# Kernel tuning notes

Measured on AMD Instinct MI355X. Metric: run time of the kernel, lower is better.

Reference implementation:

```python
import jax, jax.numpy as jnp
import numpy as np


def _rope_cache(seq_len, head_dim):
    half = head_dim // 2
    inv_freq = 1.0 / (10000.0 ** (jnp.arange(half, dtype=jnp.float32) / half))
    ang = jnp.arange(seq_len, dtype=jnp.float32)[:, None] * inv_freq[None, :]  # [S, half]
    return jnp.cos(ang), jnp.sin(ang)


def _apply_rope(x, cos, sin):
    # x: [B,H,S,D], interleaved pairs (even=x1, odd=x2)
    b, h, s, d = x.shape
    xp = x.reshape(b, h, s, d // 2, 2)
    x1, x2 = xp[..., 0], xp[..., 1]
    c = cos[:s][None, None]
    sn = sin[:s][None, None]
    o1 = x1 * c - x2 * sn
    o2 = x1 * sn + x2 * c
    return jnp.stack([o1, o2], axis=-1).reshape(b, h, s, d)


def setup_inputs() -> dict:
    key = jax.random.key(0)
    ks = jax.random.split(key, 5)
    B, N, D = 2, 2048, 2048
    sc = 0.02
    return {
        "x": jax.random.normal(ks[0], (B, N, D), jnp.float32),
        "wq": jax.random.normal(ks[1], (D, D), jnp.float32) * sc,
        "wk": jax.random.normal(ks[2], (D, D), jnp.float32) * sc,
        "wv": jax.random.normal(ks[3], (D, D), jnp.float32) * sc,
        "wo": jax.random.normal(ks[4], (D, D), jnp.float32) * sc,
    }


def reference(x, wq, wk, wv, wo):
    H = 16
    B, N, D = x.shape
    dk = D // H
    # torch nn.Linear: y = x @ W^T
    def proj(w):
        return (x @ w.T).reshape(B, N, H, dk).transpose(0, 2, 1, 3)  # [B,H,N,dk]
    Q, K, V = proj(wq), proj(wk), proj(wv)
    cos, sin = _rope_cache(N, dk)
    Q = _apply_rope(Q, cos, sin)
    K = _apply_rope(K, cos, sin)
    scores = jnp.einsum('bhnd,bhmd->bhnm', Q, K) / jnp.sqrt(jnp.float32(dk))
    causal = jnp.tril(jnp.ones((N, N), dtype=bool))
    scores = jnp.where(causal[None, None], scores, -jnp.inf)
    attn = jax.nn.softmax(scores, axis=-1)
    out = jnp.einsum('bhnm,bhmd->bhnd', attn, V)
    out = out.transpose(0, 2, 1, 3).reshape(B, N, D)
    return out @ wo.T, K, V
```

## Files before the change

kernel.cpp:

```cpp
#include <hip/hip_runtime.h>
#include <stdint.h>

typedef __bf16 bf16x8 __attribute__((ext_vector_type(8)));
typedef float f32x4 __attribute__((ext_vector_type(4)));

#define DEV __device__ __forceinline__
#define CAST_G(p) (const __attribute__((address_space(1))) unsigned int*)(p)
#define CAST_L(p) (__attribute__((address_space(3))) unsigned int*)(p)

constexpr int SEQ = 2048;
constexpr int DIM = 2048;
constexpr int NH  = 16;
constexpr int DK  = 128;
constexpr int BATCH = 2;
constexpr size_t TSZ = (size_t)BATCH * SEQ * DIM;
constexpr size_t WSZ = (size_t)DIM * DIM;
constexpr float ATTN_SCALE = 0.08838834764831845f;

DEV unsigned short f2bf(float f) {
  unsigned int u = __float_as_uint(f);
  unsigned int r = (u + 0x7fffu + ((u >> 16) & 1u)) >> 16;
  return (unsigned short)r;
}

__global__ __launch_bounds__(256)
void cvt_f32_bf16(const float* __restrict__ src, unsigned short* __restrict__ dst,
                  int n8) {
  int i = blockIdx.x * 256 + threadIdx.x;
  if (i >= n8) return;
  float4 a = *reinterpret_cast<const float4*>(src + (size_t)i * 8);
  float4 b = *reinterpret_cast<const float4*>(src + (size_t)i * 8 + 4);
  unsigned short o[8];
  o[0] = f2bf(a.x); o[1] = f2bf(a.y); o[2] = f2bf(a.z); o[3] = f2bf(a.w);
  o[4] = f2bf(b.x); o[5] = f2bf(b.y); o[6] = f2bf(b.z); o[7] = f2bf(b.w);
  *reinterpret_cast<uint4*>(dst + (size_t)i * 8) = *reinterpret_cast<const uint4*>(o);
}

template <int MODE>
__global__ __launch_bounds__(256, 2)
void gemm_rope(const unsigned short* __restrict__ A,
               const unsigned short* __restrict__ W,
               unsigned short* __restrict__ Db,
               float* __restrict__ Df) {
  __shared__ __align__(16) unsigned short As[128 * 64];
  __shared__ __align__(16) unsigned short Bs[128 * 64];

  const int t = threadIdx.x;
  const int lane = t & 63;
  const int wid = t >> 6;
  const int wr = (wid >> 1) << 6;
  const int wc = (wid & 1) << 6;
  const int l16 = lane & 15, lg = lane >> 4;
  const int row0 = blockIdx.y * 128;
  const int col0 = blockIdx.x * 128;

  const int srow = t >> 3;
  const int scol = ((t & 7) ^ (srow & 7)) << 3;
  const unsigned short* Asrc = A + (size_t)(row0 + srow) * DIM + scol;
  const unsigned short* Wsrc = W + (size_t)(col0 + srow) * DIM + scol;

  f32x4 acc[4][4] = {};

  for (int k0 = 0; k0 < DIM; k0 += 64) {
    __syncthreads();
#pragma unroll
    for (int i = 0; i < 4; ++i) {
      __builtin_amdgcn_global_load_lds(CAST_G(Asrc + (size_t)i * 32 * DIM + k0),
                                       CAST_L(As + i * 2048 + wid * 512), 16, 0, 0);
      __builtin_amdgcn_global_load_lds(CAST_G(Wsrc + (size_t)i * 32 * DIM + k0),
                                       CAST_L(Bs + i * 2048 + wid * 512), 16, 0, 0);
    }
    __syncthreads();
#pragma unroll
    for (int ks = 0; ks < 2; ++ks) {
      bf16x8 af[4], bfr[4];
#pragma unroll
      for (int i = 0; i < 4; ++i) {
        int ra = wr + i * 16 + l16;
        af[i] = *reinterpret_cast<const bf16x8*>(&As[ra * 64 + (((ks * 4 + lg) ^ (ra & 7)) << 3)]);
        int rb = wc + i * 16 + l16;
        bfr[i] = *reinterpret_cast<const bf16x8*>(&Bs[rb * 64 + (((ks * 4 + lg) ^ (rb & 7)) << 3)]);
      }
#pragma unroll
      for (int i = 0; i < 4; ++i)
#pragma unroll
        for (int j = 0; j < 4; ++j)
          acc[i][j] = __builtin_amdgcn_mfma_f32_16x16x32_bf16(af[i], bfr[j], acc[i][j], 0, 0, 0);
    }
  }

  if (MODE == 0) {
#pragma unroll
    for (int i = 0; i < 4; ++i)
#pragma unroll
      for (int j = 0; j < 4; ++j) {
        int colg = col0 + wc + j * 16 + l16;
#pragma unroll
        for (int r = 0; r < 4; ++r) {
          int rowg = row0 + wr + i * 16 + lg * 4 + r;
          Df[(size_t)rowg * DIM + colg] = acc[i][j][r];
        }
      }
  } else {
#pragma unroll
    for (int j = 0; j < 4; ++j) {
      int colg = col0 + wc + j * 16 + l16;
      int jj = (colg >> 1) & 63;
      float invf = __expf((float)jj * -0.14391156831212787f);
#pragma unroll
      for (int i = 0; i < 4; ++i) {
#pragma unroll
        for (int r = 0; r < 4; ++r) {
          int rowg = row0 + wr + i * 16 + lg * 4 + r;
          float v = acc[i][j][r];
          float outv;
          if (MODE == 1 || MODE == 2) {
            float p = __shfl_xor(v, 1, 64);
            int pos = rowg & (SEQ - 1);
            float ang = (float)pos * invf;
            float sn, cs;
            __sincosf(ang, &sn, &cs);
            outv = (colg & 1) ? fmaf(p, sn, v * cs) : fmaf(v, cs, -(p * sn));
          } else {
            outv = v;
          }
          int b = rowg >> 11, pos = rowg & (SEQ - 1);
          int h = colg >> 7, d = colg & (DK - 1);
          size_t idx = (((size_t)(b * NH + h)) * SEQ + pos) * DK + d;
          if (MODE == 1) Db[idx] = f2bf(outv);
          if (MODE == 2) { Df[idx] = outv; Db[idx] = f2bf(outv); }
          if (MODE == 3) Df[idx] = outv;
        }
      }
    }
  }
}

__global__ __launch_bounds__(256, 2)
void vtrans(const float* __restrict__ V, unsigned short* __restrict__ VT) {
  __shared__ float vs[64 * 128];
  const int t = threadIdx.x;
  const int bh = blockIdx.y;
  const int p0 = blockIdx.x * 64;
  const float* src = V + ((size_t)bh * SEQ + p0) * DK;
#pragma unroll
  for (int s = 0; s < 8; ++s) {
    int id = s * 256 + t;
    *reinterpret_cast<float4*>(&vs[id * 4]) = *reinterpret_cast<const float4*>(&src[id * 4]);
  }
  __syncthreads();
  const int w = t >> 6, l = t & 63;
  unsigned short* dstb = VT + (size_t)bh * DK * SEQ + p0;
#pragma unroll
  for (int it = 0; it < 4; ++it) {
    int d = w * 32 + (it & 1) * 16 + (l & 15);
    int kc = (it >> 1) * 4 + (l >> 4);
    unsigned short tmp[8];
#pragma unroll
    for (int j = 0; j < 8; ++j) tmp[j] = f2bf(vs[(kc * 8 + j) * DK + d]);
    *reinterpret_cast<uint4*>(&dstb[(size_t)d * SEQ + kc * 8]) =
        *reinterpret_cast<const uint4*>(tmp);
  }
}

struct __align__(16) AttnSmem {
  unsigned short Qs[128 * 128];
  unsigned short Ks[64 * 128];
  unsigned short Vts[128 * 64];
  unsigned short Ps[8 * 16 * 64];
};

__global__ __launch_bounds__(512, 1)
void attn_fused(const unsigned short* __restrict__ Q,
                const unsigned short* __restrict__ K,
                const unsigned short* __restrict__ VT,
                unsigned short* __restrict__ AO) {
  __shared__ AttnSmem sm;
  const int t = threadIdx.x;
  const int lane = t & 63;
  const int wid = t >> 6;
  const int l16 = lane & 15, lg = lane >> 4;
  const int pj = blockIdx.x;
  const int bh = blockIdx.y;
  const int b = bh >> 4, h = bh & 15;

  const unsigned short* Kbase = K + (size_t)bh * SEQ * DK;
  const unsigned short* VTbase = VT + (size_t)bh * DK * SEQ;

  for (int half = 0; half < 2; ++half) {
    const int qt = half ? pj : (15 - pj);
    const int q0 = qt * 128;
    const int nkv = 2 * (qt + 1);
    const unsigned short* Qbase = Q + ((size_t)bh * SEQ + q0) * DK;

#pragma unroll
    for (int s = 0; s < 4; ++s) {
      int id = s * 512 + t;
      int r = id >> 4, c = id & 15;
      uint4 v = *reinterpret_cast<const uint4*>(Qbase + (size_t)r * DK + (c << 3));
      *reinterpret_cast<uint4*>(&sm.Qs[r * 128 + ((c ^ (r & 7)) << 3)]) = v;
    }

    f32x4 accO[8] = {};
    float mrun[4], lrun[4];
#pragma unroll
    for (int r = 0; r < 4; ++r) { mrun[r] = -INFINITY; lrun[r] = 0.f; }

    uint4 pk[2], pv[2];
#pragma unroll
    for (int s = 0; s < 2; ++s) {
      int id = s * 512 + t;
      int rk = id >> 4, ck = id & 15;
      pk[s] = *reinterpret_cast<const uint4*>(Kbase + (size_t)rk * DK + (ck << 3));
      int rv = id >> 3, cv = id & 7;
      pv[s] = *reinterpret_cast<const uint4*>(VTbase + (size_t)rv * SEQ + (cv << 3));
    }

    for (int kt = 0; kt < nkv; ++kt) {
      const int key0 = kt * 64;
      __syncthreads();
#pragma unroll
      for (int s = 0; s < 2; ++s) {
        int id = s * 512 + t;
        int rk = id >> 4, ck = id & 15;
        *reinterpret_cast<uint4*>(&sm.Ks[rk * 128 + ((ck ^ (rk & 7)) << 3)]) = pk[s];
        int rv = id >> 3, cv = id & 7;
        *reinterpret_cast<uint4*>(&sm.Vts[rv * 64 + ((cv ^ (rv & 7)) << 3)]) = pv[s];
      }
      __syncthreads();
      if (kt + 1 < nkv) {
        const int kn = key0 + 64;
#pragma unroll
        for (int s = 0; s < 2; ++s) {
          int id = s * 512 + t;
          int rk = id >> 4, ck = id & 15;
          pk[s] = *reinterpret_cast<const uint4*>(Kbase + (size_t)(kn + rk) * DK + (ck << 3));
          int rv = id >> 3, cv = id & 7;
          pv[s] = *reinterpret_cast<const uint4*>(VTbase + (size_t)rv * SEQ + kn + (cv << 3));
        }
      }

      f32x4 sf[4] = {};
#pragma unroll
      for (int ks = 0; ks < 4; ++ks) {
        int ra = wid * 16 + l16;
        bf16x8 aq = *reinterpret_cast<const bf16x8*>(
            &sm.Qs[ra * 128 + (((ks * 4 + lg) ^ (ra & 7)) << 3)]);
#pragma unroll
        for (int nj = 0; nj < 4; ++nj) {
          int rb = nj * 16 + l16;
          bf16x8 bk = *reinterpret_cast<const bf16x8*>(
              &sm.Ks[rb * 128 + (((ks * 4 + lg) ^ (rb & 7)) << 3)]);
          sf[nj] = __builtin_amdgcn_mfma_f32_16x16x32_bf16(aq, bk, sf[nj], 0, 0, 0);
        }
      }

      const int qwbase = q0 + wid * 16;
      const bool need_mask = (key0 + 63) > qwbase;
#pragma unroll
      for (int nj = 0; nj < 4; ++nj) {
        int kcol = key0 + nj * 16 + l16;
#pragma unroll
        for (int r = 0; r < 4; ++r) {
          float v = sf[nj][r] * ATTN_SCALE;
          if (need_mask) {
            int qrow = qwbase + lg * 4 + r;
            if (kcol > qrow) v = -INFINITY;
          }
          sf[nj][r] = v;
        }
      }

      float alpha[4];
#pragma unroll
      for (int r = 0; r < 4; ++r) {
        float m0 = fmaxf(fmaxf(sf[0][r], sf[1][r]), fmaxf(sf[2][r], sf[3][r]));
#pragma unroll
        for (int off = 1; off < 16; off <<= 1)
          m0 = fmaxf(m0, __shfl_xor(m0, off, 64));
        float mn = fmaxf(mrun[r], m0);
        alpha[r] = __expf(mrun[r] - mn);
        mrun[r] = mn;
      }
      float rs[4] = {0.f, 0.f, 0.f, 0.f};
#pragma unroll
      for (int nj = 0; nj < 4; ++nj) {
        int colb = nj * 16 + l16;
        int ch = colb >> 3, cb = colb & 7;
#pragma unroll
        for (int r = 0; r < 4; ++r) {
          float p = __expf(sf[nj][r] - mrun[r]);
          rs[r] += p;
          int prow = lg * 4 + r;
          sm.Ps[wid * 1024 + prow * 64 + ((ch ^ (prow & 7)) << 3) + cb] = f2bf(p);
        }
      }
#pragma unroll
      for (int r = 0; r < 4; ++r) {
        float s0 = rs[r];
#pragma unroll
        for (int off = 1; off < 16; off <<= 1)
          s0 += __shfl_xor(s0, off, 64);
        lrun[r] = lrun[r] * alpha[r] + s0;
      }
#pragma unroll
      for (int dj = 0; dj < 8; ++dj)
#pragma unroll
        for (int r = 0; r < 4; ++r) accO[dj][r] *= alpha[r];

#pragma unroll
      for (int ks = 0; ks < 2; ++ks) {
        bf16x8 ap = *reinterpret_cast<const bf16x8*>(
            &sm.Ps[wid * 1024 + l16 * 64 + (((ks * 4 + lg) ^ (l16 & 7)) << 3)]);
#pragma unroll
        for (int dj = 0; dj < 8; ++dj) {
          int rv = dj * 16 + l16;
          bf16x8 bv = *reinterpret_cast<const bf16x8*>(
              &sm.Vts[rv * 64 + (((ks * 4 + lg) ^ (rv & 7)) << 3)]);
          accO[dj] = __builtin_amdgcn_mfma_f32_16x16x32_bf16(ap, bv, accO[dj], 0, 0, 0);
        }
      }
    }

    __syncthreads();
    unsigned short* Pw = sm.Ks + wid * 2048;
    float inv[4];
#pragma unroll
    for (int r = 0; r < 4; ++r) inv[r] = 1.0f / lrun[r];
#pragma unroll
    for (int dj = 0; dj < 8; ++dj)
#pragma unroll
      for (int r = 0; r < 4; ++r)
        Pw[(lg * 4 + r) * 128 + dj * 16 + l16] = f2bf(accO[dj][r] * inv[r]);
#pragma unroll
    for (int ps = 0; ps < 4; ++ps) {
      int row = ps * 4 + lg;
      uint4 v = *reinterpret_cast<const uint4*>(&Pw[row * 128 + l16 * 8]);
      int qpos = q0 + wid * 16 + row;
      *reinterpret_cast<uint4*>(
          &AO[((size_t)(b * SEQ + qpos)) * DIM + h * DK + l16 * 8]) = v;
    }
    __syncthreads();
  }
}

extern "C" void kernel_launch(void* const* d_in, const int* in_sizes, int n_in,
                              void* d_out, int out_size, void* d_ws, size_t ws_size,
                              hipStream_t stream) {
  const float* x  = (const float*)d_in[0];
  const float* wq = (const float*)d_in[1];
  const float* wk = (const float*)d_in[2];
  const float* wv = (const float*)d_in[3];
  const float* wo = (const float*)d_in[4];

  float* outF = (float*)d_out;
  float* outK = outF + TSZ;
  float* outV = outF + 2 * TSZ;

  unsigned short* qb = (unsigned short*)outF;
  unsigned short* kb = qb + TSZ;

  unsigned short* xb  = (unsigned short*)d_ws;
  unsigned short* aop = xb + TSZ;
  unsigned short* wb  = xb + 2 * TSZ;
  unsigned short* vtb = xb;

  dim3 blk(256);
  dim3 ggrid(16, 32);
  const int cvtW = (int)(WSZ / 2048), n8W = (int)(WSZ / 8);

  cvt_f32_bf16<<<dim3((int)(TSZ / 2048)), blk, 0, stream>>>(x, xb, (int)(TSZ / 8));

  cvt_f32_bf16<<<dim3(cvtW), blk, 0, stream>>>(wq, wb, n8W);
  gemm_rope<1><<<ggrid, blk, 0, stream>>>(xb, wb, qb, nullptr);

  cvt_f32_bf16<<<dim3(cvtW), blk, 0, stream>>>(wk, wb, n8W);
  gemm_rope<2><<<ggrid, blk, 0, stream>>>(xb, wb, kb, outK);

  cvt_f32_bf16<<<dim3(cvtW), blk, 0, stream>>>(wv, wb, n8W);
  gemm_rope<3><<<ggrid, blk, 0, stream>>>(xb, wb, nullptr, outV);

  vtrans<<<dim3(32, 32), blk, 0, stream>>>(outV, vtb);

  attn_fused<<<dim3(8, 32), dim3(512), 0, stream>>>(qb, kb, vtb, aop);

  cvt_f32_bf16<<<dim3(cvtW), blk, 0, stream>>>(wo, wb, n8W);
  gemm_rope<0><<<ggrid, blk, 0, stream>>>(aop, wb, nullptr, outF);
}
```

Baseline: 358.3 us.

## Stage 128-key K/V tiles per sync in attention and raise MFMA priority

The attention kernel now loads 128 keys of K and V^T into shared memory per stage and processes them as two 64-key sub-tiles, halving the number of barrier and global-prefetch rounds per query tile. MFMA sections are wrapped in s_setprio to favour matrix work over other waves, and the grid is transposed so that blocks of the same head-batch are launched adjacently. Shared memory grows and more prefetch registers are held per thread, which may pressure occupancy or register allocation.

```diff
diff --git a/kernel.cpp b/kernel.cpp
--- a/kernel.cpp
+++ b/kernel.cpp
@@ -165,8 +165,8 @@
 
 struct __align__(16) AttnSmem {
   unsigned short Qs[128 * 128];
-  unsigned short Ks[64 * 128];
-  unsigned short Vts[128 * 64];
+  unsigned short Ks[128 * 128];
+  unsigned short Vts[128 * 128];
   unsigned short Ps[8 * 16 * 64];
 };
 
@@ -180,8 +180,8 @@
   const int lane = t & 63;
   const int wid = t >> 6;
   const int l16 = lane & 15, lg = lane >> 4;
-  const int pj = blockIdx.x;
-  const int bh = blockIdx.y;
+  const int bh = blockIdx.x;
+  const int pj = blockIdx.y;
   const int b = bh >> 4, h = bh & 15;
 
   const unsigned short* Kbase = K + (size_t)bh * SEQ * DK;
@@ -190,7 +190,7 @@
   for (int half = 0; half < 2; ++half) {
     const int qt = half ? pj : (15 - pj);
     const int q0 = qt * 128;
-    const int nkv = 2 * (qt + 1);
+    const int nst = qt + 1;
     const unsigned short* Qbase = Q + ((size_t)bh * SEQ + q0) * DK;
 
 #pragma unroll
@@ -206,119 +206,126 @@
 #pragma unroll
     for (int r = 0; r < 4; ++r) { mrun[r] = -INFINITY; lrun[r] = 0.f; }
 
-    uint4 pk[2], pv[2];
-#pragma unroll
-    for (int s = 0; s < 2; ++s) {
+    uint4 pk[4], pv[4];
+#pragma unroll
+    for (int s = 0; s < 4; ++s) {
       int id = s * 512 + t;
       int rk = id >> 4, ck = id & 15;
       pk[s] = *reinterpret_cast<const uint4*>(Kbase + (size_t)rk * DK + (ck << 3));
-      int rv = id >> 3, cv = id & 7;
-      pv[s] = *reinterpret_cast<const uint4*>(VTbase + (size_t)rv * SEQ + (cv << 3));
-    }
-
-    for (int kt = 0; kt < nkv; ++kt) {
-      const int key0 = kt * 64;
+      pv[s] = *reinterpret_cast<const uint4*>(VTbase + (size_t)rk * SEQ + (ck << 3));
+    }
+
+    for (int kt = 0; kt < nst; ++kt) {
       __syncthreads();
 #pragma unroll
-      for (int s = 0; s < 2; ++s) {
+      for (int s = 0; s < 4; ++s) {
         int id = s * 512 + t;
         int rk = id >> 4, ck = id & 15;
-        *reinterpret_cast<uint4*>(&sm.Ks[rk * 128 + ((ck ^ (rk & 7)) << 3)]) = pk[s];
-        int rv = id >> 3, cv = id & 7;
-        *reinterpret_cast<uint4*>(&sm.Vts[rv * 64 + ((cv ^ (rv & 7)) << 3)]) = pv[s];
+        int sw = ((ck ^ (rk & 7)) << 3);
+        *reinterpret_cast<uint4*>(&sm.Ks[rk * 128 + sw]) = pk[s];
+        *reinterpret_cast<uint4*>(&sm.Vts[rk * 128 + sw]) = pv[s];
       }
       __syncthreads();
-      if (kt + 1 < nkv) {
-        const int kn = key0 + 64;
-#pragma unroll
-        for (int s = 0; s < 2; ++s) {
+      if (kt + 1 < nst) {
+        const int kn = (kt + 1) * 128;
+#pragma unroll
+        for (int s = 0; s < 4; ++s) {
           int id = s * 512 + t;
           int rk = id >> 4, ck = id & 15;
           pk[s] = *reinterpret_cast<const uint4*>(Kbase + (size_t)(kn + rk) * DK + (ck << 3));
-          int rv = id >> 3, cv = id & 7;
-          pv[s] = *reinterpret_cast<const uint4*>(VTbase + (size_t)rv * SEQ + kn + (cv << 3));
-        }
-      }
-
-      f32x4 sf[4] = {};
-#pragma unroll
-      for (int ks = 0; ks < 4; ++ks) {
-        int ra = wid * 16 + l16;
-        bf16x8 aq = *reinterpret_cast<const bf16x8*>(
-            &sm.Qs[ra * 128 + (((ks * 4 + lg) ^ (ra & 7)) << 3)]);
+          pv[s] = *reinterpret_cast<const uint4*>(VTbase + (size_t)rk * SEQ + kn + (ck << 3));
+        }
+      }
+
+#pragma unroll
+      for (int sub = 0; sub < 2; ++sub) {
+        const int key0 = kt * 128 + sub * 64;
+
+        f32x4 sf[4] = {};
+        __builtin_amdgcn_s_setprio(1);
+#pragma unroll
+        for (int ks = 0; ks < 4; ++ks) {
+          int ra = wid * 16 + l16;
+          bf16x8 aq = *reinterpret_cast<const bf16x8*>(
+              &sm.Qs[ra * 128 + (((ks * 4 + lg) ^ (ra & 7)) << 3)]);
+#pragma unroll
+          for (int nj = 0; nj < 4; ++nj) {
+            int rb = sub * 64 + nj * 16 + l16;
+            bf16x8 bk = *reinterpret_cast<const bf16x8*>(
+                &sm.Ks[rb * 128 + (((ks * 4 + lg) ^ (rb & 7)) << 3)]);
+            sf[nj] = __builtin_amdgcn_mfma_f32_16x16x32_bf16(aq, bk, sf[nj], 0, 0, 0);
+          }
+        }
+        __builtin_amdgcn_s_setprio(0);
+
+        const int qwbase = q0 + wid * 16;
+        const bool need_mask = (key0 + 63) > qwbase;
 #pragma unroll
         for (int nj = 0; nj < 4; ++nj) {
-          int rb = nj * 16 + l16;
-          bf16x8 bk = *reinterpret_cast<const bf16x8*>(
-              &sm.Ks[rb * 128 + (((ks * 4 + lg) ^ (rb & 7)) << 3)]);
-          sf[nj] = __builtin_amdgcn_mfma_f32_16x16x32_bf16(aq, bk, sf[nj], 0, 0, 0);
-        }
-      }
-
-      const int qwbase = q0 + wid * 16;
-      const bool need_mask = (key0 + 63) > qwbase;
-#pragma unroll
-      for (int nj = 0; nj < 4; ++nj) {
-        int kcol = key0 + nj * 16 + l16;
+          int kcol = key0 + nj * 16 + l16;
+#pragma unroll
+          for (int r = 0; r < 4; ++r) {
+            float v = sf[nj][r] * ATTN_SCALE;
+            if (need_mask) {
+              int qrow = qwbase + lg * 4 + r;
+              if (kcol > qrow) v = -INFINITY;
+            }
+            sf[nj][r] = v;
+          }
+        }
+
+        float alpha[4];
 #pragma unroll
         for (int r = 0; r < 4; ++r) {
-          float v = sf[nj][r] * ATTN_SCALE;
-          if (need_mask) {
-            int qrow = qwbase + lg * 4 + r;
-            if (kcol > qrow) v = -INFINITY;
-          }
-          sf[nj][r] = v;
-        }
-      }
-
-      float alpha[4];
-#pragma unroll
-      for (int r = 0; r < 4; ++r) {
-        float m0 = fmaxf(fmaxf(sf[0][r], sf[1][r]), fmaxf(sf[2][r], sf[3][r]));
-#pragma unroll
-        for (int off = 1; off < 16; off <<= 1)
-          m0 = fmaxf(m0, __shfl_xor(m0, off, 64));
-        float mn = fmaxf(mrun[r], m0);
-        alpha[r] = __expf(mrun[r] - mn);
-        mrun[r] = mn;
-      }
-      float rs[4] = {0.f, 0.f, 0.f, 0.f};
-#pragma unroll
-      for (int nj = 0; nj < 4; ++nj) {
-        int colb = nj * 16 + l16;
-        int ch = colb >> 3, cb = colb & 7;
+          float m0 = fmaxf(fmaxf(sf[0][r], sf[1][r]), fmaxf(sf[2][r], sf[3][r]));
+#pragma unroll
+          for (int off = 1; off < 16; off <<= 1)
+            m0 = fmaxf(m0, __shfl_xor(m0, off, 64));
+          float mn = fmaxf(mrun[r], m0);
+          alpha[r] = __expf(mrun[r] - mn);
+          mrun[r] = mn;
+        }
+        float rs[4] = {0.f, 0.f, 0.f, 0.f};
+#pragma unroll
+        for (int nj = 0; nj < 4; ++nj) {
+          int colb = nj * 16 + l16;
+          int ch = colb >> 3, cb = colb & 7;
+#pragma unroll
+          for (int r = 0; r < 4; ++r) {
+            float p = __expf(sf[nj][r] - mrun[r]);
+            rs[r] += p;
+            int prow = lg * 4 + r;
+            sm.Ps[wid * 1024 + prow * 64 + ((ch ^ (prow & 7)) << 3) + cb] = f2bf(p);
+          }
+        }
 #pragma unroll
         for (int r = 0; r < 4; ++r) {
-          float p = __expf(sf[nj][r] - mrun[r]);
-          rs[r] += p;
-          int prow = lg * 4 + r;
-          sm.Ps[wid * 1024 + prow * 64 + ((ch ^ (prow & 7)) << 3) + cb] = f2bf(p);
-        }
-      }
-#pragma unroll
-      for (int r = 0; r < 4; ++r) {
-        float s0 = rs[r];
-#pragma unroll
-        for (int off = 1; off < 16; off <<= 1)
-          s0 += __shfl_xor(s0, off, 64);
-        lrun[r] = lrun[r] * alpha[r] + s0;
-      }
-#pragma unroll
-      for (int dj = 0; dj < 8; ++dj)
-#pragma unroll
-        for (int r = 0; r < 4; ++r) accO[dj][r] *= alpha[r];
-
-#pragma unroll
-      for (int ks = 0; ks < 2; ++ks) {
-        bf16x8 ap = *reinterpret_cast<const bf16x8*>(
-            &sm.Ps[wid * 1024 + l16 * 64 + (((ks * 4 + lg) ^ (l16 & 7)) << 3)]);
-#pragma unroll
-        for (int dj = 0; dj < 8; ++dj) {
-          int rv = dj * 16 + l16;
-          bf16x8 bv = *reinterpret_cast<const bf16x8*>(
-              &sm.Vts[rv * 64 + (((ks * 4 + lg) ^ (rv & 7)) << 3)]);
-          accO[dj] = __builtin_amdgcn_mfma_f32_16x16x32_bf16(ap, bv, accO[dj], 0, 0, 0);
-        }
+          float s0 = rs[r];
+#pragma unroll
+          for (int off = 1; off < 16; off <<= 1)
+            s0 += __shfl_xor(s0, off, 64);
+          lrun[r] = lrun[r] * alpha[r] + s0;
+        }
+#pragma unroll
+        for (int dj = 0; dj < 8; ++dj)
+#pragma unroll
+          for (int r = 0; r < 4; ++r) accO[dj][r] *= alpha[r];
+
+        __builtin_amdgcn_s_setprio(1);
+#pragma unroll
+        for (int ks = 0; ks < 2; ++ks) {
+          bf16x8 ap = *reinterpret_cast<const bf16x8*>(
+              &sm.Ps[wid * 1024 + l16 * 64 + (((ks * 4 + lg) ^ (l16 & 7)) << 3)]);
+#pragma unroll
+          for (int dj = 0; dj < 8; ++dj) {
+            int rv = dj * 16 + l16;
+            int c = sub * 8 + ks * 4 + lg;
+            bf16x8 bv = *reinterpret_cast<const bf16x8*>(
+                &sm.Vts[rv * 128 + ((c ^ (rv & 7)) << 3)]);
+            accO[dj] = __builtin_amdgcn_mfma_f32_16x16x32_bf16(ap, bv, accO[dj], 0, 0, 0);
+          }
+        }
+        __builtin_amdgcn_s_setprio(0);
       }
     }
 
@@ -382,7 +389,7 @@
 
   vtrans<<<dim3(32, 32), blk, 0, stream>>>(outV, vtb);
 
-  attn_fused<<<dim3(8, 32), dim3(512), 0, stream>>>(qb, kb, vtb, aop);
+  attn_fused<<<dim3(32, 8), dim3(512), 0, stream>>>(qb, kb, vtb, aop);
 
   cvt_f32_bf16<<<dim3(cvtW), blk, 0, stream>>>(wo, wb, n8W);
   gemm_rope<0><<<ggrid, blk, 0, stream>>>(aop, wb, nullptr, outF);
```

After: 329.1 us. 1.09x faster.

## Split attention blocks into 256-thread halves with Q kept in registers

Applied to the files above, without the earlier changes.

The attention kernel now launches 256-thread blocks covering 64 query rows each, with a z-dimension picking which half of the 128-row tile a block owns. Q fragments are loaded straight into registers instead of staged through shared memory, which cuts LDS use and allows two blocks per CU. The grid is reordered so the head index is the fast dimension, and s_setprio is raised around the MFMA loops. In exchange, each K/V tile is loaded by twice as many blocks, which increases global and L2 traffic.

```diff
diff --git a/kernel.cpp b/kernel.cpp
--- a/kernel.cpp
+++ b/kernel.cpp
@@ -164,13 +164,12 @@
 }
 
 struct __align__(16) AttnSmem {
-  unsigned short Qs[128 * 128];
   unsigned short Ks[64 * 128];
   unsigned short Vts[128 * 64];
-  unsigned short Ps[8 * 16 * 64];
+  unsigned short Ps[4 * 16 * 64];
 };
 
-__global__ __launch_bounds__(512, 1)
+__global__ __launch_bounds__(256, 2)
 void attn_fused(const unsigned short* __restrict__ Q,
                 const unsigned short* __restrict__ K,
                 const unsigned short* __restrict__ VT,
@@ -180,8 +179,9 @@
   const int lane = t & 63;
   const int wid = t >> 6;
   const int l16 = lane & 15, lg = lane >> 4;
-  const int pj = blockIdx.x;
-  const int bh = blockIdx.y;
+  const int bh = blockIdx.x;
+  const int pj = blockIdx.y;
+  const int hb = blockIdx.z;
   const int b = bh >> 4, h = bh & 15;
 
   const unsigned short* Kbase = K + (size_t)bh * SEQ * DK;
@@ -191,25 +191,24 @@
     const int qt = half ? pj : (15 - pj);
     const int q0 = qt * 128;
     const int nkv = 2 * (qt + 1);
-    const unsigned short* Qbase = Q + ((size_t)bh * SEQ + q0) * DK;
-
-#pragma unroll
-    for (int s = 0; s < 4; ++s) {
-      int id = s * 512 + t;
-      int r = id >> 4, c = id & 15;
-      uint4 v = *reinterpret_cast<const uint4*>(Qbase + (size_t)r * DK + (c << 3));
-      *reinterpret_cast<uint4*>(&sm.Qs[r * 128 + ((c ^ (r & 7)) << 3)]) = v;
-    }
+    const int qw0 = q0 + hb * 64 + wid * 16;
+
+    const unsigned short* Qw = Q + ((size_t)bh * SEQ + qw0) * DK;
+    bf16x8 qf[4];
+#pragma unroll
+    for (int ks = 0; ks < 4; ++ks)
+      qf[ks] = *reinterpret_cast<const bf16x8*>(
+          Qw + (size_t)l16 * DK + (ks * 4 + lg) * 8);
 
     f32x4 accO[8] = {};
     float mrun[4], lrun[4];
 #pragma unroll
     for (int r = 0; r < 4; ++r) { mrun[r] = -INFINITY; lrun[r] = 0.f; }
 
-    uint4 pk[2], pv[2];
-#pragma unroll
-    for (int s = 0; s < 2; ++s) {
-      int id = s * 512 + t;
+    uint4 pk[4], pv[4];
+#pragma unroll
+    for (int s = 0; s < 4; ++s) {
+      int id = s * 256 + t;
       int rk = id >> 4, ck = id & 15;
       pk[s] = *reinterpret_cast<const uint4*>(Kbase + (size_t)rk * DK + (ck << 3));
       int rv = id >> 3, cv = id & 7;
@@ -220,8 +219,8 @@
       const int key0 = kt * 64;
       __syncthreads();
 #pragma unroll
-      for (int s = 0; s < 2; ++s) {
-        int id = s * 512 + t;
+      for (int s = 0; s < 4; ++s) {
+        int id = s * 256 + t;
         int rk = id >> 4, ck = id & 15;
         *reinterpret_cast<uint4*>(&sm.Ks[rk * 128 + ((ck ^ (rk & 7)) << 3)]) = pk[s];
         int rv = id >> 3, cv = id & 7;
@@ -231,8 +230,8 @@
       if (kt + 1 < nkv) {
         const int kn = key0 + 64;
 #pragma unroll
-        for (int s = 0; s < 2; ++s) {
-          int id = s * 512 + t;
+        for (int s = 0; s < 4; ++s) {
+          int id = s * 256 + t;
           int rk = id >> 4, ck = id & 15;
           pk[s] = *reinterpret_cast<const uint4*>(Kbase + (size_t)(kn + rk) * DK + (ck << 3));
           int rv = id >> 3, cv = id & 7;
@@ -241,22 +240,20 @@
       }
 
       f32x4 sf[4] = {};
+      __builtin_amdgcn_s_setprio(1);
 #pragma unroll
       for (int ks = 0; ks < 4; ++ks) {
-        int ra = wid * 16 + l16;
-        bf16x8 aq = *reinterpret_cast<const bf16x8*>(
-            &sm.Qs[ra * 128 + (((ks * 4 + lg) ^ (ra & 7)) << 3)]);
 #pragma unroll
         for (int nj = 0; nj < 4; ++nj) {
           int rb = nj * 16 + l16;
           bf16x8 bk = *reinterpret_cast<const bf16x8*>(
               &sm.Ks[rb * 128 + (((ks * 4 + lg) ^ (rb & 7)) << 3)]);
-          sf[nj] = __builtin_amdgcn_mfma_f32_16x16x32_bf16(aq, bk, sf[nj], 0, 0, 0);
-        }
-      }
-
-      const int qwbase = q0 + wid * 16;
-      const bool need_mask = (key0 + 63) > qwbase;
+          sf[nj] = __builtin_amdgcn_mfma_f32_16x16x32_bf16(qf[ks], bk, sf[nj], 0, 0, 0);
+        }
+      }
+      __builtin_amdgcn_s_setprio(0);
+
+      const bool need_mask = (key0 + 63) > qw0;
 #pragma unroll
       for (int nj = 0; nj < 4; ++nj) {
         int kcol = key0 + nj * 16 + l16;
@@ -264,7 +261,7 @@
         for (int r = 0; r < 4; ++r) {
           float v = sf[nj][r] * ATTN_SCALE;
           if (need_mask) {
-            int qrow = qwbase + lg * 4 + r;
+            int qrow = qw0 + lg * 4 + r;
             if (kcol > qrow) v = -INFINITY;
           }
           sf[nj][r] = v;
@@ -308,6 +305,7 @@
 #pragma unroll
         for (int r = 0; r < 4; ++r) accO[dj][r] *= alpha[r];
 
+      __builtin_amdgcn_s_setprio(1);
 #pragma unroll
       for (int ks = 0; ks < 2; ++ks) {
         bf16x8 ap = *reinterpret_cast<const bf16x8*>(
@@ -320,6 +318,7 @@
           accO[dj] = __builtin_amdgcn_mfma_f32_16x16x32_bf16(ap, bv, accO[dj], 0, 0, 0);
         }
       }
+      __builtin_amdgcn_s_setprio(0);
     }
 
     __syncthreads();
@@ -336,7 +335,7 @@
     for (int ps = 0; ps < 4; ++ps) {
       int row = ps * 4 + lg;
       uint4 v = *reinterpret_cast<const uint4*>(&Pw[row * 128 + l16 * 8]);
-      int qpos = q0 + wid * 16 + row;
+      int qpos = qw0 + row;
       *reinterpret_cast<uint4*>(
           &AO[((size_t)(b * SEQ + qpos)) * DIM + h * DK + l16 * 8]) = v;
     }
@@ -382,7 +381,7 @@
 
   vtrans<<<dim3(32, 32), blk, 0, stream>>>(outV, vtb);
 
-  attn_fused<<<dim3(8, 32), dim3(512), 0, stream>>>(qb, kb, vtb, aop);
+  attn_fused<<<dim3(32, 8, 2), blk, 0, stream>>>(qb, kb, vtb, aop);
 
   cvt_f32_bf16<<<dim3(cvtW), blk, 0, stream>>>(wo, wb, n8W);
   gemm_rope<0><<<ggrid, blk, 0, stream>>>(aop, wb, nullptr, outF);
```

After: 408.4 us. 1.14x slower.
